# Performance work log

Measured on AMD Instinct MI355X. Metric: run time of the kernel, lower is better.

## Reference

```python
import jax, jax.numpy as jnp
import numpy as np

NV = 40962      # vertices at mesh level 6 (10*4^6 + 2)
NV_PREV = 10242 # vertices at mesh level 5
GROUPS = 32
EPS = 1e-5


def setup_inputs() -> dict:
    key = jax.random.key(0)
    ks = jax.random.split(key, 8)
    B, Cin, Cout, K = 8, 64, 64, 7
    x = jax.random.normal(ks[0], (B, Cin, NV_PREV), dtype=jnp.float32)
    L_val = jax.random.normal(ks[1], (NV, K), dtype=jnp.float32)
    EW_val = jax.random.normal(ks[2], (NV, K), dtype=jnp.float32)
    NS_val = jax.random.normal(ks[3], (NV, K), dtype=jnp.float32)
    coeffs = jax.random.normal(ks[4], (Cout, Cin, 4), dtype=jnp.float32) * 0.05
    bias = jax.random.normal(ks[5], (Cout,), dtype=jnp.float32) * 0.05
    gamma = jnp.ones((Cout,), dtype=jnp.float32)
    beta = jnp.zeros((Cout,), dtype=jnp.float32)
    nbr_idx = jax.random.randint(ks[6], (NV, K), 0, NV, dtype=jnp.int32)
    return {"x": x, "L_val": L_val, "EW_val": EW_val, "NS_val": NS_val,
            "coeffs": coeffs, "bias": bias, "gamma": gamma, "beta": beta,
            "nbr_idx": nbr_idx}


def reference(x, L_val, EW_val, NS_val, coeffs, bias, gamma, beta, nbr_idx):
    B, Cin, nvp = x.shape
    nv = nbr_idx.shape[0]
    # --- MeshConvTranspose: zero-pad upsample (old vertices are a prefix) ---
    up = jnp.zeros((B, Cin, nv), x.dtype).at[:, :, :nvp].set(x)
    # --- irregular neighbor gather: [B, Cin, nv, 7] ---
    g = up[:, :, nbr_idx]
    # sparse operator applications (shared gather, three weighted sums)
    lap = jnp.einsum('bcvk,vk->bcv', g, L_val)
    ew = jnp.einsum('bcvk,vk->bcv', g, EW_val)
    ns = jnp.einsum('bcvk,vk->bcv', g, NS_val)
    feat = jnp.stack([up, lap, ew, ns], axis=2)  # [B, Cin, 4, nv]
    # learned linear combination over (in_channels, 4 operators)
    out = jnp.einsum('oik,bikv->bov', coeffs, feat) + bias[None, :, None]
    # --- GroupNorm(32, Cout) ---
    Cout = out.shape[1]
    og = out.reshape(B, GROUPS, (Cout // GROUPS) * nv)
    mean = og.mean(axis=-1, keepdims=True)
    var = og.var(axis=-1, keepdims=True)
    og = (og - mean) * jax.lax.rsqrt(var + EPS)
    out = og.reshape(B, Cout, nv) * gamma[None, :, None] + beta[None, :, None]
    # --- ReLU ---
    return jax.nn.relu(out)
```

## Files before the change

kernel.cpp:

```cpp
#include <hip/hip_runtime.h>
#include <hip/hip_bf16.h>

#define NVV    40962
#define NVP    10242
#define BB     8
#define CIN    64
#define COUT   64
#define KK     7
#define EPSV   1e-5f

#define VT     64
#define NTILE  641
#define KDIM   256

typedef __attribute__((ext_vector_type(8))) short short8;
typedef __attribute__((ext_vector_type(4))) float floatx4;

__device__ __forceinline__ unsigned f2bf(float f) {
    unsigned u = __builtin_bit_cast(unsigned, f);
    return (u + 0x7FFFu + ((u >> 16) & 1u)) >> 16;
}
__device__ __forceinline__ unsigned pk2(float a, float b) {
    __hip_bfloat162 h = __float22bfloat162_rn(make_float2(a, b));
    unsigned r;
    __builtin_memcpy(&r, &h, 4);
    return r;
}


__global__ __launch_bounds__(256) void k_prep(const float* __restrict__ coeffs,
                                              unsigned short* __restrict__ cW) {
    for (int t = threadIdx.x; t < COUT * KDIM; t += 256)
        cW[t] = (unsigned short)f2bf(coeffs[t]);
}

__global__ __launch_bounds__(256) void k_tr(const float* __restrict__ x,
                                            float* __restrict__ xT) {
    __shared__ float tile[64][65];
    const int b    = blockIdx.y;
    const int v0   = blockIdx.x * 64;
    const int lane = threadIdx.x & 63;
    const int wave = threadIdx.x >> 6;
    const int v    = v0 + lane;
    #pragma unroll
    for (int r = 0; r < 16; ++r) {
        int i = wave * 16 + r;
        tile[i][lane] = (v < NVP) ? x[((size_t)b * CIN + i) * NVP + v] : 0.f;
    }
    __syncthreads();
    #pragma unroll
    for (int r = 0; r < 16; ++r) {
        int vv = wave * 16 + r;
        if (v0 + vv < NVP)
            xT[((size_t)b * NVP + v0 + vv) * 64 + lane] = tile[lane][vv];
    }
}

__global__ __launch_bounds__(256, 4) void k_conv(
    const float* __restrict__ xT,
    const float* __restrict__ Lw,
    const float* __restrict__ Ew,
    const float* __restrict__ Nw,
    const unsigned short* __restrict__ cW,
    const float* __restrict__ bias,
    const int*   __restrict__ nbr,
    float* __restrict__ out,
    float* __restrict__ stats)
{
    __shared__ unsigned short Fbuf[VT * 256];
    __shared__ float sred[4][4][4];

    const int bid   = blockIdx.x;
    const int b     = bid & 7;
    const int tile  = bid >> 3;
    const int vbase = tile * VT;
    const int tid   = threadIdx.x;
    const int wave  = tid >> 6;
    const int lane  = tid & 63;
    const int q     = lane >> 4;
    const int l15   = lane & 15;

    {
        const int v  = lane;
        const int ic = wave;
        const int vg = vbase + v;
        const bool va = (vg < NVV);
        int jj[KK]; float wl[KK], we[KK], wn[KK];
        #pragma unroll
        for (int k = 0; k < KK; ++k) { jj[k] = NVP; wl[k] = we[k] = wn[k] = 0.f; }
        if (va) {
            #pragma unroll
            for (int k = 0; k < KK; ++k) {
                jj[k] = nbr[vg * KK + k];
                wl[k] = Lw[vg * KK + k];
                we[k] = Ew[vg * KK + k];
                wn[k] = Nw[vg * KK + k];
            }
        }
        const float* xTb = xT + (size_t)b * NVP * 64 + ic * 16;
        float u[16], l[16], e[16], n[16];
        #pragma unroll
        for (int t = 0; t < 16; ++t) { u[t] = l[t] = e[t] = n[t] = 0.f; }
        if (vg < NVP) {
            const float* p = xTb + (size_t)vg * 64;
            #pragma unroll
            for (int s = 0; s < 4; ++s) {
                float4 t = *(const float4*)(p + 4 * s);
                u[4*s] = t.x; u[4*s+1] = t.y; u[4*s+2] = t.z; u[4*s+3] = t.w;
            }
        }
        #pragma unroll
        for (int k = 0; k < KK; ++k) {
            const int j = jj[k];
            if (j < NVP) {
                const float* p = xTb + (size_t)j * 64;
                const float a = wl[k], bb2 = we[k], c2 = wn[k];
                #pragma unroll
                for (int s = 0; s < 4; ++s) {
                    float4 t = *(const float4*)(p + 4 * s);
                    l[4*s]   = fmaf(t.x, a, l[4*s]);   e[4*s]   = fmaf(t.x, bb2, e[4*s]);   n[4*s]   = fmaf(t.x, c2, n[4*s]);
                    l[4*s+1] = fmaf(t.y, a, l[4*s+1]); e[4*s+1] = fmaf(t.y, bb2, e[4*s+1]); n[4*s+1] = fmaf(t.y, c2, n[4*s+1]);
                    l[4*s+2] = fmaf(t.z, a, l[4*s+2]); e[4*s+2] = fmaf(t.z, bb2, e[4*s+2]); n[4*s+2] = fmaf(t.z, c2, n[4*s+2]);
                    l[4*s+3] = fmaf(t.w, a, l[4*s+3]); e[4*s+3] = fmaf(t.w, bb2, e[4*s+3]); n[4*s+3] = fmaf(t.w, c2, n[4*s+3]);
                }
            }
        }
        #pragma unroll
        for (int jg = 0; jg < 8; ++jg) {
            const int i0 = 2 * jg;
            uint4 w;
            w.x = pk2(u[i0],   l[i0]);
            w.y = pk2(e[i0],   n[i0]);
            w.z = pk2(u[i0+1], l[i0+1]);
            w.w = pk2(e[i0+1], n[i0+1]);
            const int g    = ic * 8 + jg;
            const int phys = g ^ (v & 31);
            *(uint4*)(Fbuf + v * 256 + phys * 8) = w;
        }
    }
    __syncthreads();

    short8 afrag[8];
    {
        const unsigned short* wrow = cW + (16 * wave + l15) * KDIM + q * 8;
        #pragma unroll
        for (int k0 = 0; k0 < 8; ++k0)
            afrag[k0] = *(const short8*)(wrow + k0 * 32);
    }

    floatx4 acc[4] = {{0,0,0,0},{0,0,0,0},{0,0,0,0},{0,0,0,0}};
    #pragma unroll
    for (int k0 = 0; k0 < 8; ++k0) {
        #pragma unroll
        for (int nt = 0; nt < 4; ++nt) {
            const int row  = nt * 16 + l15;
            const int phys = (k0 * 4 + q) ^ (row & 31);
            const short8 bfrag = *(const short8*)(Fbuf + row * 256 + phys * 8);
            acc[nt] = __builtin_amdgcn_mfma_f32_16x16x32_bf16(afrag[k0], bfrag, acc[nt], 0, 0, 0);
        }
    }

    float bs[4];
    #pragma unroll
    for (int r = 0; r < 4; ++r) bs[r] = bias[16 * wave + q * 4 + r];

    float cv[4][4];
    float sA = 0.f, s2A = 0.f, sB = 0.f, s2B = 0.f;
    #pragma unroll
    for (int nt = 0; nt < 4; ++nt) {
        const bool ok = (vbase + nt * 16 + l15 < NVV);
        #pragma unroll
        for (int r = 0; r < 4; ++r) {
            float c = acc[nt][r] + bs[r];
            cv[nt][r] = c;
            if (ok) {
                if (r < 2) { sA += c; s2A = fmaf(c, c, s2A); }
                else       { sB += c; s2B = fmaf(c, c, s2B); }
            }
        }
    }
    #pragma unroll
    for (int m = 1; m < 16; m <<= 1) {
        sA  += __shfl_xor(sA,  m);
        s2A += __shfl_xor(s2A, m);
        sB  += __shfl_xor(sB,  m);
        s2B += __shfl_xor(s2B, m);
    }
    if (l15 == 0) {
        sred[wave][q][0] = sA; sred[wave][q][1] = s2A;
        sred[wave][q][2] = sB; sred[wave][q][3] = s2B;
    }
    __syncthreads();

    float* outT = (float*)Fbuf;
    #pragma unroll
    for (int nt = 0; nt < 4; ++nt)
        #pragma unroll
        for (int r = 0; r < 4; ++r)
            outT[(16 * wave + 4 * q + r) * 68 + nt * 16 + l15] = cv[nt][r];
    __syncthreads();

    const bool okS = (vbase + lane < NVV);
    float* ob = out + ((size_t)b * COUT + 16 * wave) * NVV + vbase + lane;
    #pragma unroll
    for (int oo = 0; oo < 16; ++oo) {
        float val = outT[(16 * wave + oo) * 68 + lane];
        if (okS) ob[(size_t)oo * NVV] = val;
    }

    if (tid < 64) {
        const int w = tid >> 4, qq = (tid >> 2) & 3, e = tid & 3;
        const int g = 8 * w + 2 * qq + (e >> 1);
        atomicAdd(&stats[b * 64 + 2 * g + (e & 1)], sred[w][qq][e]);
    }
}

__global__ __launch_bounds__(256) void k_norm(
    float* __restrict__ out,
    const float* __restrict__ stats,
    const float* __restrict__ gamma,
    const float* __restrict__ beta)
{
    const int row  = blockIdx.x >> 1;
    const int half = blockIdx.x & 1;
    const int o = row & (COUT - 1);
    const int b = row >> 6;
    const int g = o >> 1;
    const float inv_cnt = 1.f / (float)(2 * NVV);
    const float mean = stats[b * 64 + 2 * g] * inv_cnt;
    const float var  = fmaf(stats[b * 64 + 2 * g + 1], inv_cnt, -mean * mean);
    const float rs   = rsqrtf(var + EPSV);
    const float sc   = gamma[o] * rs;
    const float sh   = fmaf(-mean, sc, beta[o]);

    const int HALF = NVV / 4;
    const int c0   = half * HALF;
    const int cEnd = half ? (NVV / 2) : HALF;
    float2* p = (float2*)(out + (size_t)row * NVV);
    #pragma unroll 4
    for (int c = c0 + (int)threadIdx.x; c < cEnd; c += 256) {
        float2 val = p[c];
        float y0 = fmaf(val.x, sc, sh);
        float y1 = fmaf(val.y, sc, sh);
        val.x = y0 > 0.f ? y0 : 0.f;
        val.y = y1 > 0.f ? y1 : 0.f;
        p[c] = val;
    }
}

extern "C" void kernel_launch(void* const* d_in, const int* in_sizes, int n_in,
                              void* d_out, int out_size, void* d_ws, size_t ws_size,
                              hipStream_t stream) {
    const float* x      = (const float*)d_in[0];
    const float* Lw     = (const float*)d_in[1];
    const float* Ew     = (const float*)d_in[2];
    const float* Nw     = (const float*)d_in[3];
    const float* coeffs = (const float*)d_in[4];
    const float* bias   = (const float*)d_in[5];
    const float* gamma  = (const float*)d_in[6];
    const float* beta   = (const float*)d_in[7];
    const int*   nbr    = (const int*)d_in[8];
    float* out   = (float*)d_out;
    float*          stats = (float*)d_ws;
    unsigned short* cW    = (unsigned short*)((char*)d_ws + 2048);
    float*          xT    = (float*)((char*)d_ws + 36864);

    (void)hipMemsetAsync(stats, 0, BB * 64 * sizeof(float), stream);

    k_prep<<<dim3(1), dim3(256), 0, stream>>>(coeffs, cW);

    k_tr<<<dim3(161, BB), dim3(256), 0, stream>>>(x, xT);

    k_conv<<<dim3(BB * NTILE), dim3(256), 0, stream>>>(xT, Lw, Ew, Nw, cW, bias, nbr, out, stats);

    k_norm<<<dim3(2 * BB * COUT), dim3(256), 0, stream>>>(out, stats, gamma, beta);
}
```

Before: 213.2 us.

## Store transposed input and pre-norm output in bf16, fold prep into transpose

The transposed input is now stored as bf16, which halves gather traffic in the conv kernel. All neighbor loads are issued before the FMAs. The conv output goes to a bf16 scratch buffer, and the norm kernel reads it and writes fp32 to the output, so the fp32 intermediate round trip is gone. The memset and coeff-prep launches are folded into the transpose kernel to cut launch count. The cost is an extra bf16 rounding of the pre-norm activations and the input, which may reduce accuracy.

Result: faster. 201.6 us (-5.5%).

```diff
diff --git a/kernel.cpp b/kernel.cpp
--- a/kernel.cpp
+++ b/kernel.cpp
@@ -9,9 +9,14 @@
 #define KK     7
 #define EPSV   1e-5f
 
-#define VT     64
-#define NTILE  641
-#define KDIM   256
+#define VT      64
+#define NTILE   641
+#define KDIM    256
+#define PSTRIDE 40968
+
+#define CW_OFF  2048
+#define XT_OFF  36864
+#define PRE_OFF 10524672
 
 typedef __attribute__((ext_vector_type(8))) short short8;
 typedef __attribute__((ext_vector_type(4))) float floatx4;
@@ -26,16 +31,14 @@
     __builtin_memcpy(&r, &h, 4);
     return r;
 }
-
-
-__global__ __launch_bounds__(256) void k_prep(const float* __restrict__ coeffs,
-                                              unsigned short* __restrict__ cW) {
-    for (int t = threadIdx.x; t < COUT * KDIM; t += 256)
-        cW[t] = (unsigned short)f2bf(coeffs[t]);
-}
+__device__ __forceinline__ float bflo(unsigned u) { return __builtin_bit_cast(float, u << 16); }
+__device__ __forceinline__ float bfhi(unsigned u) { return __builtin_bit_cast(float, u & 0xffff0000u); }
 
 __global__ __launch_bounds__(256) void k_tr(const float* __restrict__ x,
-                                            float* __restrict__ xT) {
+                                            unsigned short* __restrict__ xT,
+                                            const float* __restrict__ coeffs,
+                                            unsigned short* __restrict__ cW,
+                                            float* __restrict__ stats) {
     __shared__ float tile[64][65];
     const int b    = blockIdx.y;
     const int v0   = blockIdx.x * 64;
@@ -47,24 +50,32 @@
         int i = wave * 16 + r;
         tile[i][lane] = (v < NVP) ? x[((size_t)b * CIN + i) * NVP + v] : 0.f;
     }
+    if (blockIdx.x == 0 && b == 0) {
+        for (int t = threadIdx.x; t < 512; t += 256) stats[t] = 0.f;
+        for (int t = threadIdx.x; t < COUT * KDIM; t += 256)
+            cW[t] = (unsigned short)f2bf(coeffs[t]);
+    }
     __syncthreads();
-    #pragma unroll
-    for (int r = 0; r < 16; ++r) {
-        int vv = wave * 16 + r;
-        if (v0 + vv < NVP)
-            xT[((size_t)b * NVP + v0 + vv) * 64 + lane] = tile[lane][vv];
+    const int i2 = lane & 31;
+    #pragma unroll
+    for (int r = 0; r < 8; ++r) {
+        int vv = wave * 16 + 2 * r + (lane >> 5);
+        if (v0 + vv < NVP) {
+            unsigned w = pk2(tile[2 * i2][vv], tile[2 * i2 + 1][vv]);
+            ((unsigned*)(xT + ((size_t)b * NVP + v0 + vv) * 64))[i2] = w;
+        }
     }
 }
 
 __global__ __launch_bounds__(256, 4) void k_conv(
-    const float* __restrict__ xT,
+    const unsigned short* __restrict__ xT,
     const float* __restrict__ Lw,
     const float* __restrict__ Ew,
     const float* __restrict__ Nw,
     const unsigned short* __restrict__ cW,
     const float* __restrict__ bias,
     const int*   __restrict__ nbr,
-    float* __restrict__ out,
+    unsigned short* __restrict__ pre,
     float* __restrict__ stats)
 {
     __shared__ unsigned short Fbuf[VT * 256];
@@ -97,41 +108,47 @@
                 wn[k] = Nw[vg * KK + k];
             }
         }
-        const float* xTb = xT + (size_t)b * NVP * 64 + ic * 16;
-        float u[16], l[16], e[16], n[16];
-        #pragma unroll
-        for (int t = 0; t < 16; ++t) { u[t] = l[t] = e[t] = n[t] = 0.f; }
+        const unsigned short* xTb = xT + (size_t)b * NVP * 64 + ic * 16;
+
+        uint4 ga[KK], gb[KK], gu0, gu1;
+        gu0 = gu1 = make_uint4(0, 0, 0, 0);
+        #pragma unroll
+        for (int k = 0; k < KK; ++k) { ga[k] = make_uint4(0,0,0,0); gb[k] = make_uint4(0,0,0,0); }
         if (vg < NVP) {
-            const float* p = xTb + (size_t)vg * 64;
+            const uint4* p = (const uint4*)(xTb + (size_t)vg * 64);
+            gu0 = p[0]; gu1 = p[1];
+        }
+        #pragma unroll
+        for (int k = 0; k < KK; ++k) {
+            if (jj[k] < NVP) {
+                const uint4* p = (const uint4*)(xTb + (size_t)jj[k] * 64);
+                ga[k] = p[0]; gb[k] = p[1];
+            }
+        }
+
+        float l[16], e[16], n[16];
+        #pragma unroll
+        for (int t = 0; t < 16; ++t) { l[t] = e[t] = n[t] = 0.f; }
+        #pragma unroll
+        for (int k = 0; k < KK; ++k) {
+            const float a = wl[k], bb2 = we[k], c2 = wn[k];
+            const unsigned uu[8] = { ga[k].x, ga[k].y, ga[k].z, ga[k].w,
+                                     gb[k].x, gb[k].y, gb[k].z, gb[k].w };
             #pragma unroll
-            for (int s = 0; s < 4; ++s) {
-                float4 t = *(const float4*)(p + 4 * s);
-                u[4*s] = t.x; u[4*s+1] = t.y; u[4*s+2] = t.z; u[4*s+3] = t.w;
-            }
-        }
-        #pragma unroll
-        for (int k = 0; k < KK; ++k) {
-            const int j = jj[k];
-            if (j < NVP) {
-                const float* p = xTb + (size_t)j * 64;
-                const float a = wl[k], bb2 = we[k], c2 = wn[k];
-                #pragma unroll
-                for (int s = 0; s < 4; ++s) {
-                    float4 t = *(const float4*)(p + 4 * s);
-                    l[4*s]   = fmaf(t.x, a, l[4*s]);   e[4*s]   = fmaf(t.x, bb2, e[4*s]);   n[4*s]   = fmaf(t.x, c2, n[4*s]);
-                    l[4*s+1] = fmaf(t.y, a, l[4*s+1]); e[4*s+1] = fmaf(t.y, bb2, e[4*s+1]); n[4*s+1] = fmaf(t.y, c2, n[4*s+1]);
-                    l[4*s+2] = fmaf(t.z, a, l[4*s+2]); e[4*s+2] = fmaf(t.z, bb2, e[4*s+2]); n[4*s+2] = fmaf(t.z, c2, n[4*s+2]);
-                    l[4*s+3] = fmaf(t.w, a, l[4*s+3]); e[4*s+3] = fmaf(t.w, bb2, e[4*s+3]); n[4*s+3] = fmaf(t.w, c2, n[4*s+3]);
-                }
-            }
-        }
+            for (int j2 = 0; j2 < 8; ++j2) {
+                float f0 = bflo(uu[j2]), f1 = bfhi(uu[j2]);
+                l[2*j2]   = fmaf(f0, a,  l[2*j2]);   e[2*j2]   = fmaf(f0, bb2, e[2*j2]);   n[2*j2]   = fmaf(f0, c2, n[2*j2]);
+                l[2*j2+1] = fmaf(f1, a,  l[2*j2+1]); e[2*j2+1] = fmaf(f1, bb2, e[2*j2+1]); n[2*j2+1] = fmaf(f1, c2, n[2*j2+1]);
+            }
+        }
+        const unsigned uup[8] = { gu0.x, gu0.y, gu0.z, gu0.w, gu1.x, gu1.y, gu1.z, gu1.w };
         #pragma unroll
         for (int jg = 0; jg < 8; ++jg) {
             const int i0 = 2 * jg;
             uint4 w;
-            w.x = pk2(u[i0],   l[i0]);
+            w.x = pk2(bflo(uup[jg]), l[i0]);
             w.y = pk2(e[i0],   n[i0]);
-            w.z = pk2(u[i0+1], l[i0+1]);
+            w.z = pk2(bfhi(uup[jg]) , l[i0+1]);
             w.w = pk2(e[i0+1], n[i0+1]);
             const int g    = ic * 8 + jg;
             const int phys = g ^ (v & 31);
@@ -200,12 +217,16 @@
             outT[(16 * wave + 4 * q + r) * 68 + nt * 16 + l15] = cv[nt][r];
     __syncthreads();
 
-    const bool okS = (vbase + lane < NVV);
-    float* ob = out + ((size_t)b * COUT + 16 * wave) * NVV + vbase + lane;
-    #pragma unroll
-    for (int oo = 0; oo < 16; ++oo) {
-        float val = outT[(16 * wave + oo) * 68 + lane];
-        if (okS) ob[(size_t)oo * NVV] = val;
+    if (lane < 32) {
+        const int vloc = 2 * lane;
+        if (vbase + vloc < NVV) {
+            unsigned short* prow = pre + (size_t)(b * COUT + 16 * wave) * PSTRIDE + vbase;
+            #pragma unroll
+            for (int oo = 0; oo < 16; ++oo) {
+                float2 t = *(const float2*)(outT + (16 * wave + oo) * 68 + vloc);
+                *(unsigned*)(prow + (size_t)oo * PSTRIDE + vloc) = pk2(t.x, t.y);
+            }
+        }
     }
 
     if (tid < 64) {
@@ -216,13 +237,14 @@
 }
 
 __global__ __launch_bounds__(256) void k_norm(
+    const unsigned short* __restrict__ pre,
     float* __restrict__ out,
     const float* __restrict__ stats,
     const float* __restrict__ gamma,
     const float* __restrict__ beta)
 {
-    const int row  = blockIdx.x >> 1;
-    const int half = blockIdx.x & 1;
+    const int row     = blockIdx.x >> 2;
+    const int quarter = blockIdx.x & 3;
     const int o = row & (COUT - 1);
     const int b = row >> 6;
     const int g = o >> 1;
@@ -233,18 +255,28 @@
     const float sc   = gamma[o] * rs;
     const float sh   = fmaf(-mean, sc, beta[o]);
 
-    const int HALF = NVV / 4;
-    const int c0   = half * HALF;
-    const int cEnd = half ? (NVV / 2) : HALF;
-    float2* p = (float2*)(out + (size_t)row * NVV);
-    #pragma unroll 4
-    for (int c = c0 + (int)threadIdx.x; c < cEnd; c += 256) {
-        float2 val = p[c];
-        float y0 = fmaf(val.x, sc, sh);
-        float y1 = fmaf(val.y, sc, sh);
-        val.x = y0 > 0.f ? y0 : 0.f;
-        val.y = y1 > 0.f ? y1 : 0.f;
-        p[c] = val;
+    const uint4* src = (const uint4*)(pre + (size_t)row * PSTRIDE);
+    float* orow = out + (size_t)row * NVV;
+    #pragma unroll
+    for (int it = 0; it < 5; ++it) {
+        const int c = quarter * 1280 + it * 256 + (int)threadIdx.x;
+        uint4 u = src[c];
+        float f[8] = { bflo(u.x), bfhi(u.x), bflo(u.y), bfhi(u.y),
+                       bflo(u.z), bfhi(u.z), bflo(u.w), bfhi(u.w) };
+        float* p = orow + 8 * c;
+        #pragma unroll
+        for (int t = 0; t < 4; ++t) {
+            float y0 = fmaf(f[2*t],   sc, sh);
+            float y1 = fmaf(f[2*t+1], sc, sh);
+            float2 v2 = make_float2(y0 > 0.f ? y0 : 0.f, y1 > 0.f ? y1 : 0.f);
+            *(float2*)(p + 2 * t) = v2;
+        }
+    }
+    if (quarter == 3 && threadIdx.x == 0) {
+        unsigned u = *(const unsigned*)(pre + (size_t)row * PSTRIDE + 40960);
+        float y0 = fmaf(bflo(u), sc, sh);
+        float y1 = fmaf(bfhi(u), sc, sh);
+        *(float2*)(orow + 40960) = make_float2(y0 > 0.f ? y0 : 0.f, y1 > 0.f ? y1 : 0.f);
     }
 }
 
@@ -260,18 +292,15 @@
     const float* gamma  = (const float*)d_in[6];
     const float* beta   = (const float*)d_in[7];
     const int*   nbr    = (const int*)d_in[8];
-    float* out   = (float*)d_out;
+    float* out = (float*)d_out;
     float*          stats = (float*)d_ws;
-    unsigned short* cW    = (unsigned short*)((char*)d_ws + 2048);
-    float*          xT    = (float*)((char*)d_ws + 36864);
-
-    (void)hipMemsetAsync(stats, 0, BB * 64 * sizeof(float), stream);
-
-    k_prep<<<dim3(1), dim3(256), 0, stream>>>(coeffs, cW);
-
-    k_tr<<<dim3(161, BB), dim3(256), 0, stream>>>(x, xT);
-
-    k_conv<<<dim3(BB * NTILE), dim3(256), 0, stream>>>(xT, Lw, Ew, Nw, cW, bias, nbr, out, stats);
-
-    k_norm<<<dim3(2 * BB * COUT), dim3(256), 0, stream>>>(out, stats, gamma, beta);
-}
+    unsigned short* cW    = (unsigned short*)((char*)d_ws + CW_OFF);
+    unsigned short* xT    = (unsigned short*)((char*)d_ws + XT_OFF);
+    unsigned short* pre   = (unsigned short*)((char*)d_ws + PRE_OFF);
+
+    k_tr<<<dim3(161, BB), dim3(256), 0, stream>>>(x, xT, coeffs, cW, stats);
+
+    k_conv<<<dim3(BB * NTILE), dim3(256), 0, stream>>>(xT, Lw, Ew, Nw, cW, bias, nbr, pre, stats);
+
+    k_norm<<<dim3(4 * BB * COUT), dim3(256), 0, stream>>>(pre, out, stats, gamma, beta);
+}
```
